# Optimization experiments

Measured on AMD Instinct MI355X. Metric: run time of the kernel, lower is better.

The kernel has to match this reference:

```python
import jax, jax.numpy as jnp
import numpy as np

WS = 8          # window size (Wh = Ww = 8)
N = WS * WS     # tokens per window = 64
DIM = 256
HEADS = 8
HEAD_DIM = DIM // HEADS
BW = 8192       # num_windows * batch


def _relative_position_index(ws: int) -> np.ndarray:
    ch, cw = np.meshgrid(np.arange(ws), np.arange(ws), indexing='ij')
    coords = np.stack([ch, cw]).reshape(2, -1)                 # (2, N)
    rel = coords[:, :, None] - coords[:, None, :]              # (2, N, N)
    rel = rel.transpose(1, 2, 0).astype(np.int32)              # (N, N, 2)
    rel[:, :, 0] += ws - 1
    rel[:, :, 1] += ws - 1
    rel[:, :, 0] *= 2 * ws - 1
    return rel.sum(-1)                                         # (N, N)


def setup_inputs() -> dict:
    key = jax.random.key(0)
    k1, k2, k3, k4, k5, k6 = jax.random.split(key, 6)
    table_size = (2 * WS - 1) * (2 * WS - 1)                   # 225
    return {
        'x': jax.random.normal(k1, (BW, N, DIM), dtype=jnp.float32),
        'w_qkv': jax.random.normal(k2, (3 * DIM, DIM), dtype=jnp.float32) * 0.02,
        'b_qkv': jax.random.normal(k3, (3 * DIM,), dtype=jnp.float32) * 0.02,
        'w_proj': jax.random.normal(k4, (DIM, DIM), dtype=jnp.float32) * 0.02,
        'b_proj': jax.random.normal(k5, (DIM,), dtype=jnp.float32) * 0.02,
        'rpb_table': jax.random.normal(k6, (table_size, HEADS), dtype=jnp.float32) * 0.02,
        'rpi': jnp.asarray(_relative_position_index(WS)),      # (N, N) int32
    }


def reference(x, w_qkv, b_qkv, w_proj, b_proj, rpb_table, rpi):
    b_, n, c = x.shape
    scale = HEAD_DIM ** (-0.5)
    qkv = x @ w_qkv.T + b_qkv                                  # (b_, n, 3c)
    qkv = qkv.reshape(b_, n, 3, HEADS, HEAD_DIM).transpose(2, 0, 3, 1, 4)
    q, k, v = qkv[0], qkv[1], qkv[2]                           # each (b_, H, n, d)
    attn = jnp.einsum('bhnd,bhmd->bhnm', q * scale, k)         # (b_, H, n, n)
    bias = rpb_table[rpi.reshape(-1)].reshape(n, n, HEADS)     # (n, n, H)
    attn = attn + bias.transpose(2, 0, 1)[None]                # + (1, H, n, n)
    attn = jax.nn.softmax(attn, axis=-1)
    out = jnp.einsum('bhnm,bhmd->bhnd', attn, v)               # (b_, H, n, d)
    out = out.transpose(0, 2, 1, 3).reshape(b_, n, c)
    return out @ w_proj.T + b_proj
```

## Files before the change

### kernel.cpp

```cpp
#include <hip/hip_runtime.h>
#include <hip/hip_bf16.h>

typedef __bf16 bf16x8 __attribute__((ext_vector_type(8)));
typedef float f32x4 __attribute__((ext_vector_type(4)));
typedef unsigned short u16;
typedef u16 u16x4 __attribute__((ext_vector_type(4)));
typedef u16 u16x8 __attribute__((ext_vector_type(8)));

__device__ __forceinline__ u16 bfbits(float f) {
  return __builtin_bit_cast(u16, (__bf16)f);
}

__global__ void wattn_prep(const float* __restrict__ wq, const float* __restrict__ wp,
                           const float* __restrict__ rpb, const int* __restrict__ rpi,
                           u16* __restrict__ wqb, u16* __restrict__ wpb,
                           float* __restrict__ biasb) {
  int i = blockIdx.x * blockDim.x + threadIdx.x;
  if (i < 196608) wqb[i] = bfbits(wq[i]);
  if (i < 65536)  wpb[i] = bfbits(wp[i]);
  if (i < 32768) {
    int h = i >> 12, nm = i & 4095;
    biasb[i] = rpb[rpi[nm] * 8 + h];
  }
}

__global__ __launch_bounds__(512, 4)
void wattn_main(const float* __restrict__ x,
                const u16* __restrict__ wq, const float* __restrict__ bq,
                const u16* __restrict__ wp, const float* __restrict__ bp,
                const float* __restrict__ bias,
                float* __restrict__ out) {
  extern __shared__ u16 sm[];
  u16* Xb = sm;
  u16* Vt = sm + 16896;

  const int b    = blockIdx.x;
  const int tid  = threadIdx.x;
  const int w    = tid >> 6;
  const int lane = tid & 63;
  const int g    = lane >> 4;
  const int li   = lane & 15;
  const int hc   = 32 * w;

  {
    const float4* xg = (const float4*)(x + (size_t)b * 16384);
    #pragma unroll
    for (int i = 0; i < 8; ++i) {
      int idx = tid + i * 512;
      float4 v = xg[idx];
      int n = idx >> 6, c = (idx & 63) * 4;
      u16x4 h;
      h[0] = bfbits(v.x); h[1] = bfbits(v.y); h[2] = bfbits(v.z); h[3] = bfbits(v.w);
      *(u16x4*)(Xb + n * 264 + c) = h;
    }
  }
  __syncthreads();

  const int xoff = li * 264 + 8 * g;

  f32x4 av[2][4];
  #pragma unroll
  for (int mt = 0; mt < 2; ++mt)
    #pragma unroll
    for (int nt = 0; nt < 4; ++nt) av[mt][nt] = f32x4{0,0,0,0};
  #pragma unroll 2
  for (int ks = 0; ks < 8; ++ks) {
    bf16x8 xb[4];
    #pragma unroll
    for (int nt = 0; nt < 4; ++nt)
      xb[nt] = *(const bf16x8*)(Xb + xoff + nt * (16 * 264) + 32 * ks);
    #pragma unroll
    for (int mt = 0; mt < 2; ++mt) {
      bf16x8 wf = *(const bf16x8*)(wq + (512 + hc + 16 * mt + li) * 256 + 32 * ks + 8 * g);
      #pragma unroll
      for (int nt = 0; nt < 4; ++nt)
        av[mt][nt] = __builtin_amdgcn_mfma_f32_16x16x32_bf16(wf, xb[nt], av[mt][nt], 0, 0, 0);
    }
  }
  {
    u16* VtW = Vt + w * 2304;
    #pragma unroll
    for (int mt = 0; mt < 2; ++mt)
      #pragma unroll
      for (int e = 0; e < 4; ++e) {
        float bb = bq[512 + hc + 16 * mt + 4 * g + e];
        #pragma unroll
        for (int nt = 0; nt < 4; ++nt)
          VtW[(16 * mt + 4 * g + e) * 72 + 16 * nt + li] = bfbits(av[mt][nt][e] + bb);
      }
  }
  __builtin_amdgcn_sched_barrier(0);

  const float scale = 0.17677669529663687f;
  bf16x8 qf[4];
  {
    f32x4 aq[2][4];
    #pragma unroll
    for (int mt = 0; mt < 2; ++mt)
      #pragma unroll
      for (int nt = 0; nt < 4; ++nt) aq[mt][nt] = f32x4{0,0,0,0};
    #pragma unroll 2
    for (int ks = 0; ks < 8; ++ks) {
      bf16x8 xb[4];
      #pragma unroll
      for (int nt = 0; nt < 4; ++nt)
        xb[nt] = *(const bf16x8*)(Xb + xoff + nt * (16 * 264) + 32 * ks);
      #pragma unroll
      for (int mt = 0; mt < 2; ++mt) {
        bf16x8 wf = *(const bf16x8*)(wq + (hc + 16 * mt + li) * 256 + 32 * ks + 8 * g);
        #pragma unroll
        for (int nt = 0; nt < 4; ++nt)
          aq[mt][nt] = __builtin_amdgcn_mfma_f32_16x16x32_bf16(wf, xb[nt], aq[mt][nt], 0, 0, 0);
      }
    }
    #pragma unroll
    for (int j = 0; j < 8; ++j) {
      int d = (j < 4) ? (4 * g + j) : (16 + 4 * g + (j - 4));
      float bb = bq[hc + d];
      #pragma unroll
      for (int t = 0; t < 4; ++t)
        qf[t][j] = (__bf16)(((j < 4 ? aq[0][t][j] : aq[1][t][j - 4]) + bb) * scale);
    }
  }
  __builtin_amdgcn_sched_barrier(0);

  bf16x8 kf[4];
  {
    f32x4 ak[2][4];
    #pragma unroll
    for (int mt = 0; mt < 2; ++mt)
      #pragma unroll
      for (int nt = 0; nt < 4; ++nt) ak[mt][nt] = f32x4{0,0,0,0};
    #pragma unroll 2
    for (int ks = 0; ks < 8; ++ks) {
      bf16x8 xb[4];
      #pragma unroll
      for (int nt = 0; nt < 4; ++nt)
        xb[nt] = *(const bf16x8*)(Xb + xoff + nt * (16 * 264) + 32 * ks);
      #pragma unroll
      for (int mt = 0; mt < 2; ++mt) {
        bf16x8 wf = *(const bf16x8*)(wq + (256 + hc + 16 * mt + li) * 256 + 32 * ks + 8 * g);
        #pragma unroll
        for (int nt = 0; nt < 4; ++nt)
          ak[mt][nt] = __builtin_amdgcn_mfma_f32_16x16x32_bf16(wf, xb[nt], ak[mt][nt], 0, 0, 0);
      }
    }
    #pragma unroll
    for (int j = 0; j < 8; ++j) {
      int d = (j < 4) ? (4 * g + j) : (16 + 4 * g + (j - 4));
      float bb = bq[256 + hc + d];
      #pragma unroll
      for (int t = 0; t < 4; ++t)
        kf[t][j] = (__bf16)((j < 4 ? ak[0][t][j] : ak[1][t][j - 4]) + bb);
    }
  }
  __builtin_amdgcn_sched_barrier(0);

  bf16x8 pa[4][2];
  {
    const float* bh = bias + w * 4096;
    #pragma unroll
    for (int ct = 0; ct < 4; ++ct) {
      f32x4 s4[4];
      #pragma unroll
      for (int rt = 0; rt < 4; ++rt)
        s4[rt] = __builtin_amdgcn_mfma_f32_16x16x32_bf16(kf[rt], qf[ct], f32x4{0,0,0,0}, 0, 0, 0);
      const float* bq_row = bh + (16 * ct + li) * 64 + 4 * g;
      float mx = -1e30f;
      #pragma unroll
      for (int rt = 0; rt < 4; ++rt) {
        f32x4 bv = *(const f32x4*)(bq_row + 16 * rt);
        #pragma unroll
        for (int e = 0; e < 4; ++e) {
          s4[rt][e] += bv[e];
          mx = fmaxf(mx, s4[rt][e]);
        }
      }
      mx = fmaxf(mx, __shfl_xor(mx, 16));
      mx = fmaxf(mx, __shfl_xor(mx, 32));
      float sum = 0.f;
      #pragma unroll
      for (int rt = 0; rt < 4; ++rt)
        #pragma unroll
        for (int e = 0; e < 4; ++e) {
          float p = __expf(s4[rt][e] - mx);
          s4[rt][e] = p;
          sum += p;
        }
      sum += __shfl_xor(sum, 16);
      sum += __shfl_xor(sum, 32);
      float rs = 1.0f / sum;
      #pragma unroll
      for (int kk = 0; kk < 2; ++kk)
        #pragma unroll
        for (int j = 0; j < 8; ++j)
          pa[ct][kk][j] = (__bf16)((j < 4 ? s4[2 * kk][j] : s4[2 * kk + 1][j - 4]) * rs);
      __builtin_amdgcn_sched_barrier(0);
    }
  }

  f32x4 o[4][2];
  #pragma unroll
  for (int mt = 0; mt < 4; ++mt)
    #pragma unroll
    for (int nt = 0; nt < 2; ++nt) o[mt][nt] = f32x4{0,0,0,0};
  {
    const u16* VtW = Vt + w * 2304;
    #pragma unroll
    for (int kk = 0; kk < 2; ++kk) {
      bf16x8 vb[2];
      #pragma unroll
      for (int nt = 0; nt < 2; ++nt) {
        const u16* row = VtW + (16 * nt + li) * 72;
        u16x4 lo = *(const u16x4*)(row + 32 * kk + 4 * g);
        u16x4 hi = *(const u16x4*)(row + 32 * kk + 16 + 4 * g);
        u16x8 cc;
        #pragma unroll
        for (int j = 0; j < 4; ++j) { cc[j] = lo[j]; cc[4 + j] = hi[j]; }
        vb[nt] = __builtin_bit_cast(bf16x8, cc);
      }
      #pragma unroll
      for (int mt = 0; mt < 4; ++mt)
        #pragma unroll
        for (int nt = 0; nt < 2; ++nt)
          o[mt][nt] = __builtin_amdgcn_mfma_f32_16x16x32_bf16(pa[mt][kk], vb[nt], o[mt][nt], 0, 0, 0);
    }
  }

  __syncthreads();
  u16* ao = sm;
  #pragma unroll
  for (int mt = 0; mt < 4; ++mt)
    #pragma unroll
    for (int nt = 0; nt < 2; ++nt)
      #pragma unroll
      for (int e = 0; e < 4; ++e)
        ao[(16 * mt + 4 * g + e) * 264 + hc + 16 * nt + li] = bfbits(o[mt][nt][e]);
  __syncthreads();

  f32x4 c2[4][2];
  #pragma unroll
  for (int rt = 0; rt < 4; ++rt)
    #pragma unroll
    for (int ct = 0; ct < 2; ++ct) c2[rt][ct] = f32x4{0,0,0,0};
  #pragma unroll 2
  for (int ks = 0; ks < 8; ++ks) {
    bf16x8 af[4];
    #pragma unroll
    for (int rt = 0; rt < 4; ++rt)
      af[rt] = *(const bf16x8*)(ao + xoff + rt * (16 * 264) + 32 * ks);
    bf16x8 wf[2];
    #pragma unroll
    for (int ct = 0; ct < 2; ++ct)
      wf[ct] = *(const bf16x8*)(wp + (32 * w + 16 * ct + li) * 256 + 32 * ks + 8 * g);
    #pragma unroll
    for (int rt = 0; rt < 4; ++rt)
      #pragma unroll
      for (int ct = 0; ct < 2; ++ct)
        c2[rt][ct] = __builtin_amdgcn_mfma_f32_16x16x32_bf16(af[rt], wf[ct], c2[rt][ct], 0, 0, 0);
  }
  {
    float* og = out + (size_t)b * 16384;
    #pragma unroll
    for (int ct = 0; ct < 2; ++ct) {
      int col = 32 * w + 16 * ct + li;
      float bpv = bp[col];
      #pragma unroll
      for (int rt = 0; rt < 4; ++rt)
        #pragma unroll
        for (int e = 0; e < 4; ++e)
          og[(16 * rt + 4 * g + e) * 256 + col] = c2[rt][ct][e] + bpv;
    }
  }
}

extern "C" void kernel_launch(void* const* d_in, const int* in_sizes, int n_in,
                              void* d_out, int out_size, void* d_ws, size_t ws_size,
                              hipStream_t stream) {
  const float* x   = (const float*)d_in[0];
  const float* wqv = (const float*)d_in[1];
  const float* bq  = (const float*)d_in[2];
  const float* wpr = (const float*)d_in[3];
  const float* bp  = (const float*)d_in[4];
  const float* rpb = (const float*)d_in[5];
  const int*   rpi = (const int*)d_in[6];
  float* out = (float*)d_out;

  u16*   wqb   = (u16*)d_ws;
  u16*   wpb   = wqb + 196608;
  float* biasb = (float*)(wpb + 65536);

  wattn_prep<<<384, 512, 0, stream>>>(wqv, wpr, rpb, rpi, wqb, wpb, biasb);

  const size_t smem = (16896 + 18432) * sizeof(u16);
  hipFuncSetAttribute(reinterpret_cast<const void*>(wattn_main),
                      hipFuncAttributeMaxDynamicSharedMemorySize, (int)smem);
  wattn_main<<<8192, 512, smem, stream>>>(x, wqb, bq, wpb, bp, biasb, out);
}
```

Before: 704.1 us.

## Keep V in registers via swapped MFMA operands, drop V LDS buffer

The V projection is now computed with X as the A operand and weights as B, so its accumulator layout matches the B-operand fragment needed by the P·V MFMA. V stays in registers instead of being written transposed to LDS and read back. This removes the V LDS buffer (shared memory per block roughly halves) and raises the launch-bounds occupancy hint from 4 to 6 blocks. It also moves the V projection after Q/K and removes a per-tile scheduling barrier in softmax. The risk is more register pressure, since V fragments stay live across the softmax, and possible spills under the tighter launch bound.

```diff
diff --git a/kernel.cpp b/kernel.cpp
--- a/kernel.cpp
+++ b/kernel.cpp
@@ -5,7 +5,6 @@
 typedef float f32x4 __attribute__((ext_vector_type(4)));
 typedef unsigned short u16;
 typedef u16 u16x4 __attribute__((ext_vector_type(4)));
-typedef u16 u16x8 __attribute__((ext_vector_type(8)));
 
 __device__ __forceinline__ u16 bfbits(float f) {
   return __builtin_bit_cast(u16, (__bf16)f);
@@ -24,7 +23,7 @@
   }
 }
 
-__global__ __launch_bounds__(512, 4)
+__global__ __launch_bounds__(512, 6)
 void wattn_main(const float* __restrict__ x,
                 const u16* __restrict__ wq, const float* __restrict__ bq,
                 const u16* __restrict__ wp, const float* __restrict__ bp,
@@ -32,7 +31,6 @@
                 float* __restrict__ out) {
   extern __shared__ u16 sm[];
   u16* Xb = sm;
-  u16* Vt = sm + 16896;
 
   const int b    = blockIdx.x;
   const int tid  = threadIdx.x;
@@ -57,41 +55,8 @@
   __syncthreads();
 
   const int xoff = li * 264 + 8 * g;
-
-  f32x4 av[2][4];
-  #pragma unroll
-  for (int mt = 0; mt < 2; ++mt)
-    #pragma unroll
-    for (int nt = 0; nt < 4; ++nt) av[mt][nt] = f32x4{0,0,0,0};
-  #pragma unroll 2
-  for (int ks = 0; ks < 8; ++ks) {
-    bf16x8 xb[4];
-    #pragma unroll
-    for (int nt = 0; nt < 4; ++nt)
-      xb[nt] = *(const bf16x8*)(Xb + xoff + nt * (16 * 264) + 32 * ks);
-    #pragma unroll
-    for (int mt = 0; mt < 2; ++mt) {
-      bf16x8 wf = *(const bf16x8*)(wq + (512 + hc + 16 * mt + li) * 256 + 32 * ks + 8 * g);
-      #pragma unroll
-      for (int nt = 0; nt < 4; ++nt)
-        av[mt][nt] = __builtin_amdgcn_mfma_f32_16x16x32_bf16(wf, xb[nt], av[mt][nt], 0, 0, 0);
-    }
-  }
-  {
-    u16* VtW = Vt + w * 2304;
-    #pragma unroll
-    for (int mt = 0; mt < 2; ++mt)
-      #pragma unroll
-      for (int e = 0; e < 4; ++e) {
-        float bb = bq[512 + hc + 16 * mt + 4 * g + e];
-        #pragma unroll
-        for (int nt = 0; nt < 4; ++nt)
-          VtW[(16 * mt + 4 * g + e) * 72 + 16 * nt + li] = bfbits(av[mt][nt][e] + bb);
-      }
-  }
-  __builtin_amdgcn_sched_barrier(0);
-
   const float scale = 0.17677669529663687f;
+
   bf16x8 qf[4];
   {
     f32x4 aq[2][4];
@@ -152,6 +117,39 @@
       #pragma unroll
       for (int t = 0; t < 4; ++t)
         kf[t][j] = (__bf16)((j < 4 ? ak[0][t][j] : ak[1][t][j - 4]) + bb);
+    }
+  }
+  __builtin_amdgcn_sched_barrier(0);
+
+  bf16x8 vb[2][2];
+  {
+    f32x4 av[4][2];
+    #pragma unroll
+    for (int mt = 0; mt < 4; ++mt)
+      #pragma unroll
+      for (int nt = 0; nt < 2; ++nt) av[mt][nt] = f32x4{0,0,0,0};
+    #pragma unroll 2
+    for (int ks = 0; ks < 8; ++ks) {
+      bf16x8 xb[4];
+      #pragma unroll
+      for (int mt = 0; mt < 4; ++mt)
+        xb[mt] = *(const bf16x8*)(Xb + xoff + mt * (16 * 264) + 32 * ks);
+      #pragma unroll
+      for (int nt = 0; nt < 2; ++nt) {
+        bf16x8 wf = *(const bf16x8*)(wq + (512 + hc + 16 * nt + li) * 256 + 32 * ks + 8 * g);
+        #pragma unroll
+        for (int mt = 0; mt < 4; ++mt)
+          av[mt][nt] = __builtin_amdgcn_mfma_f32_16x16x32_bf16(xb[mt], wf, av[mt][nt], 0, 0, 0);
+      }
+    }
+    #pragma unroll
+    for (int nt = 0; nt < 2; ++nt) {
+      float bb = bq[512 + hc + 16 * nt + li];
+      #pragma unroll
+      for (int kk = 0; kk < 2; ++kk)
+        #pragma unroll
+        for (int j = 0; j < 8; ++j)
+          vb[kk][nt][j] = (__bf16)((j < 4 ? av[2 * kk][nt][j] : av[2 * kk + 1][nt][j - 4]) + bb);
     }
   }
   __builtin_amdgcn_sched_barrier(0);
@@ -195,37 +193,22 @@
         #pragma unroll
         for (int j = 0; j < 8; ++j)
           pa[ct][kk][j] = (__bf16)((j < 4 ? s4[2 * kk][j] : s4[2 * kk + 1][j - 4]) * rs);
-      __builtin_amdgcn_sched_barrier(0);
-    }
-  }
+    }
+  }
+  __builtin_amdgcn_sched_barrier(0);
 
   f32x4 o[4][2];
   #pragma unroll
   for (int mt = 0; mt < 4; ++mt)
     #pragma unroll
     for (int nt = 0; nt < 2; ++nt) o[mt][nt] = f32x4{0,0,0,0};
-  {
-    const u16* VtW = Vt + w * 2304;
-    #pragma unroll
-    for (int kk = 0; kk < 2; ++kk) {
-      bf16x8 vb[2];
-      #pragma unroll
-      for (int nt = 0; nt < 2; ++nt) {
-        const u16* row = VtW + (16 * nt + li) * 72;
-        u16x4 lo = *(const u16x4*)(row + 32 * kk + 4 * g);
-        u16x4 hi = *(const u16x4*)(row + 32 * kk + 16 + 4 * g);
-        u16x8 cc;
-        #pragma unroll
-        for (int j = 0; j < 4; ++j) { cc[j] = lo[j]; cc[4 + j] = hi[j]; }
-        vb[nt] = __builtin_bit_cast(bf16x8, cc);
-      }
-      #pragma unroll
-      for (int mt = 0; mt < 4; ++mt)
-        #pragma unroll
-        for (int nt = 0; nt < 2; ++nt)
-          o[mt][nt] = __builtin_amdgcn_mfma_f32_16x16x32_bf16(pa[mt][kk], vb[nt], o[mt][nt], 0, 0, 0);
-    }
-  }
+  #pragma unroll
+  for (int kk = 0; kk < 2; ++kk)
+    #pragma unroll
+    for (int mt = 0; mt < 4; ++mt)
+      #pragma unroll
+      for (int nt = 0; nt < 2; ++nt)
+        o[mt][nt] = __builtin_amdgcn_mfma_f32_16x16x32_bf16(pa[mt][kk], vb[kk][nt], o[mt][nt], 0, 0, 0);
 
   __syncthreads();
   u16* ao = sm;
@@ -292,7 +275,7 @@
 
   wattn_prep<<<384, 512, 0, stream>>>(wqv, wpr, rpb, rpi, wqb, wpb, biasb);
 
-  const size_t smem = (16896 + 18432) * sizeof(u16);
+  const size_t smem = 16896 * sizeof(u16);
   hipFuncSetAttribute(reinterpret_cast<const void*>(wattn_main),
                       hipFuncAttributeMaxDynamicSharedMemorySize, (int)smem);
   wattn_main<<<8192, 512, smem, stream>>>(x, wqb, bq, wpb, bp, biasb, out);
```

New measurement: 1.165 ms. +65.4%, slower.

## Split fused window attention into attention and projection kernels via bf16 workspace

Applied to the files above, without the earlier changes.

Splits the single fused kernel into an attention kernel that writes a bf16 per-window output to global workspace and a separate projection kernel that reads it back. The attention kernel keeps V in registers instead of LDS, folds biases into accumulator initialization, and raises the occupancy target to 6 blocks per CU with smaller shared memory. This trades extra global traffic (a bf16 write and read of the intermediate, about 256 MB) for lower register and LDS pressure and higher occupancy. The original fused kernel remains as a fallback when the workspace is too small.

```diff
diff --git a/kernel.cpp b/kernel.cpp
--- a/kernel.cpp
+++ b/kernel.cpp
@@ -24,15 +24,13 @@
   }
 }
 
-__global__ __launch_bounds__(512, 4)
-void wattn_main(const float* __restrict__ x,
+__global__ __launch_bounds__(512, 6)
+void wattn_attn(const float* __restrict__ x,
                 const u16* __restrict__ wq, const float* __restrict__ bq,
-                const u16* __restrict__ wp, const float* __restrict__ bp,
                 const float* __restrict__ bias,
-                float* __restrict__ out) {
+                u16* __restrict__ ao) {
   extern __shared__ u16 sm[];
   u16* Xb = sm;
-  u16* Vt = sm + 16896;
 
   const int b    = blockIdx.x;
   const int tid  = threadIdx.x;
@@ -57,6 +55,231 @@
   __syncthreads();
 
   const int xoff = li * 264 + 8 * g;
+  const float scale = 0.17677669529663687f;
+
+  bf16x8 kf[4];
+  {
+    f32x4 ak[2][4];
+    #pragma unroll
+    for (int mt = 0; mt < 2; ++mt) {
+      f32x4 bkv = *(const f32x4*)(bq + 256 + hc + 16 * mt + 4 * g);
+      #pragma unroll
+      for (int nt = 0; nt < 4; ++nt) ak[mt][nt] = bkv;
+    }
+    #pragma unroll 1
+    for (int ks = 0; ks < 8; ++ks) {
+      bf16x8 xb[4];
+      #pragma unroll
+      for (int nt = 0; nt < 4; ++nt)
+        xb[nt] = *(const bf16x8*)(Xb + xoff + nt * (16 * 264) + 32 * ks);
+      #pragma unroll
+      for (int mt = 0; mt < 2; ++mt) {
+        bf16x8 wf = *(const bf16x8*)(wq + (256 + hc + 16 * mt + li) * 256 + 32 * ks + 8 * g);
+        #pragma unroll
+        for (int nt = 0; nt < 4; ++nt)
+          ak[mt][nt] = __builtin_amdgcn_mfma_f32_16x16x32_bf16(wf, xb[nt], ak[mt][nt], 0, 0, 0);
+      }
+    }
+    #pragma unroll
+    for (int j = 0; j < 8; ++j)
+      #pragma unroll
+      for (int t = 0; t < 4; ++t)
+        kf[t][j] = (__bf16)(j < 4 ? ak[0][t][j] : ak[1][t][j - 4]);
+  }
+  __builtin_amdgcn_sched_barrier(0);
+
+  bf16x8 vb[2][2];
+  #pragma unroll 1
+  for (int nt = 0; nt < 2; ++nt) {
+    f32x4 av[4];
+    {
+      float bb = bq[512 + hc + 16 * nt + li];
+      #pragma unroll
+      for (int mt = 0; mt < 4; ++mt) av[mt] = f32x4{bb, bb, bb, bb};
+    }
+    #pragma unroll 1
+    for (int ks = 0; ks < 8; ++ks) {
+      bf16x8 wf = *(const bf16x8*)(wq + (512 + hc + 16 * nt + li) * 256 + 32 * ks + 8 * g);
+      #pragma unroll
+      for (int mt = 0; mt < 4; ++mt) {
+        bf16x8 xb = *(const bf16x8*)(Xb + xoff + mt * (16 * 264) + 32 * ks);
+        av[mt] = __builtin_amdgcn_mfma_f32_16x16x32_bf16(xb, wf, av[mt], 0, 0, 0);
+      }
+    }
+    #pragma unroll
+    for (int kk = 0; kk < 2; ++kk)
+      #pragma unroll
+      for (int j = 0; j < 8; ++j)
+        vb[kk][nt][j] = (__bf16)(j < 4 ? av[2 * kk][j] : av[2 * kk + 1][j - 4]);
+    __builtin_amdgcn_sched_barrier(0);
+  }
+
+  bf16x8 qf[4];
+  #pragma unroll 1
+  for (int mt = 0; mt < 2; ++mt) {
+    f32x4 aq[4];
+    {
+      f32x4 bqv = *(const f32x4*)(bq + hc + 16 * mt + 4 * g);
+      #pragma unroll
+      for (int nt = 0; nt < 4; ++nt) aq[nt] = bqv;
+    }
+    #pragma unroll 1
+    for (int ks = 0; ks < 8; ++ks) {
+      bf16x8 wf = *(const bf16x8*)(wq + (hc + 16 * mt + li) * 256 + 32 * ks + 8 * g);
+      #pragma unroll
+      for (int nt = 0; nt < 4; ++nt) {
+        bf16x8 xb = *(const bf16x8*)(Xb + xoff + nt * (16 * 264) + 32 * ks);
+        aq[nt] = __builtin_amdgcn_mfma_f32_16x16x32_bf16(wf, xb, aq[nt], 0, 0, 0);
+      }
+    }
+    #pragma unroll
+    for (int t = 0; t < 4; ++t)
+      #pragma unroll
+      for (int j = 0; j < 4; ++j)
+        qf[t][4 * mt + j] = (__bf16)(aq[t][j] * scale);
+    __builtin_amdgcn_sched_barrier(0);
+  }
+
+  u16* aog = ao + (size_t)b * 16384;
+  const float* bh = bias + w * 4096;
+  #pragma unroll 1
+  for (int ct = 0; ct < 4; ++ct) {
+    const float* br = bh + (16 * ct + li) * 64 + 4 * g;
+    f32x4 s4[4];
+    #pragma unroll
+    for (int rt = 0; rt < 4; ++rt)
+      s4[rt] = __builtin_amdgcn_mfma_f32_16x16x32_bf16(kf[rt], qf[ct],
+                                                       *(const f32x4*)(br + 16 * rt), 0, 0, 0);
+    float mx = -1e30f;
+    #pragma unroll
+    for (int rt = 0; rt < 4; ++rt)
+      #pragma unroll
+      for (int e = 0; e < 4; ++e) mx = fmaxf(mx, s4[rt][e]);
+    mx = fmaxf(mx, __shfl_xor(mx, 16));
+    mx = fmaxf(mx, __shfl_xor(mx, 32));
+    float sum = 0.f;
+    #pragma unroll
+    for (int rt = 0; rt < 4; ++rt)
+      #pragma unroll
+      for (int e = 0; e < 4; ++e) {
+        float p = __expf(s4[rt][e] - mx);
+        s4[rt][e] = p;
+        sum += p;
+      }
+    sum += __shfl_xor(sum, 16);
+    sum += __shfl_xor(sum, 32);
+    float rs = 1.0f / sum;
+    bf16x8 pa0, pa1;
+    #pragma unroll
+    for (int j = 0; j < 8; ++j) {
+      pa0[j] = (__bf16)((j < 4 ? s4[0][j] : s4[1][j - 4]) * rs);
+      pa1[j] = (__bf16)((j < 4 ? s4[2][j] : s4[3][j - 4]) * rs);
+    }
+    #pragma unroll
+    for (int nt = 0; nt < 2; ++nt) {
+      f32x4 o = __builtin_amdgcn_mfma_f32_16x16x32_bf16(pa0, vb[0][nt], f32x4{0, 0, 0, 0}, 0, 0, 0);
+      o = __builtin_amdgcn_mfma_f32_16x16x32_bf16(pa1, vb[1][nt], o, 0, 0, 0);
+      #pragma unroll
+      for (int e = 0; e < 4; ++e)
+        aog[(16 * ct + 4 * g + e) * 256 + hc + 16 * nt + li] = bfbits(o[e]);
+    }
+    __builtin_amdgcn_sched_barrier(0);
+  }
+}
+
+__global__ __launch_bounds__(512, 6)
+void wattn_proj(const u16* __restrict__ ao, const u16* __restrict__ wp,
+                const float* __restrict__ bp, float* __restrict__ out) {
+  extern __shared__ u16 sm[];
+  const int b    = blockIdx.x;
+  const int tid  = threadIdx.x;
+  const int w    = tid >> 6;
+  const int lane = tid & 63;
+  const int g    = lane >> 4;
+  const int li   = lane & 15;
+
+  {
+    const u16x8* src = (const u16x8*)(ao + (size_t)b * 16384);
+    #pragma unroll
+    for (int i = 0; i < 4; ++i) {
+      int idx = tid + i * 512;
+      u16x8 v = src[idx];
+      int row = idx >> 5, c = (idx & 31) * 8;
+      *(u16x8*)(sm + row * 264 + c) = v;
+    }
+  }
+  __syncthreads();
+
+  const int xoff = li * 264 + 8 * g;
+  f32x4 c2[4][2];
+  #pragma unroll
+  for (int c = 0; c < 2; ++c) {
+    float bb = bp[32 * w + 16 * c + li];
+    #pragma unroll
+    for (int rt = 0; rt < 4; ++rt) c2[rt][c] = f32x4{bb, bb, bb, bb};
+  }
+  #pragma unroll 1
+  for (int ks = 0; ks < 8; ++ks) {
+    bf16x8 af[4];
+    #pragma unroll
+    for (int rt = 0; rt < 4; ++rt)
+      af[rt] = *(const bf16x8*)(sm + xoff + rt * (16 * 264) + 32 * ks);
+    #pragma unroll
+    for (int c = 0; c < 2; ++c) {
+      bf16x8 wf = *(const bf16x8*)(wp + (32 * w + 16 * c + li) * 256 + 32 * ks + 8 * g);
+      #pragma unroll
+      for (int rt = 0; rt < 4; ++rt)
+        c2[rt][c] = __builtin_amdgcn_mfma_f32_16x16x32_bf16(af[rt], wf, c2[rt][c], 0, 0, 0);
+    }
+  }
+  {
+    float* og = out + (size_t)b * 16384;
+    #pragma unroll
+    for (int c = 0; c < 2; ++c) {
+      int col = 32 * w + 16 * c + li;
+      #pragma unroll
+      for (int rt = 0; rt < 4; ++rt)
+        #pragma unroll
+        for (int e = 0; e < 4; ++e)
+          og[(16 * rt + 4 * g + e) * 256 + col] = c2[rt][c][e];
+    }
+  }
+}
+
+__global__ __launch_bounds__(512, 4)
+void wattn_fused(const float* __restrict__ x,
+                 const u16* __restrict__ wq, const float* __restrict__ bq,
+                 const u16* __restrict__ wp, const float* __restrict__ bp,
+                 const float* __restrict__ bias,
+                 float* __restrict__ out) {
+  extern __shared__ u16 sm[];
+  u16* Xb = sm;
+  u16* Vt = sm + 16896;
+
+  const int b    = blockIdx.x;
+  const int tid  = threadIdx.x;
+  const int w    = tid >> 6;
+  const int lane = tid & 63;
+  const int g    = lane >> 4;
+  const int li   = lane & 15;
+  const int hc   = 32 * w;
+
+  {
+    const float4* xg = (const float4*)(x + (size_t)b * 16384);
+    #pragma unroll
+    for (int i = 0; i < 8; ++i) {
+      int idx = tid + i * 512;
+      float4 v = xg[idx];
+      int n = idx >> 6, c = (idx & 63) * 4;
+      u16x4 h;
+      h[0] = bfbits(v.x); h[1] = bfbits(v.y); h[2] = bfbits(v.z); h[3] = bfbits(v.w);
+      *(u16x4*)(Xb + n * 264 + c) = h;
+    }
+  }
+  __syncthreads();
+
+  const int xoff = li * 264 + 8 * g;
+  const float scale = 0.17677669529663687f;
 
   f32x4 av[2][4];
   #pragma unroll
@@ -91,7 +314,6 @@
   }
   __builtin_amdgcn_sched_barrier(0);
 
-  const float scale = 0.17677669529663687f;
   bf16x8 qf[4];
   {
     f32x4 aq[2][4];
@@ -208,7 +430,7 @@
     const u16* VtW = Vt + w * 2304;
     #pragma unroll
     for (int kk = 0; kk < 2; ++kk) {
-      bf16x8 vb[2];
+      bf16x8 vbf[2];
       #pragma unroll
       for (int nt = 0; nt < 2; ++nt) {
         const u16* row = VtW + (16 * nt + li) * 72;
@@ -217,13 +439,13 @@
         u16x8 cc;
         #pragma unroll
         for (int j = 0; j < 4; ++j) { cc[j] = lo[j]; cc[4 + j] = hi[j]; }
-        vb[nt] = __builtin_bit_cast(bf16x8, cc);
+        vbf[nt] = __builtin_bit_cast(bf16x8, cc);
       }
       #pragma unroll
       for (int mt = 0; mt < 4; ++mt)
         #pragma unroll
         for (int nt = 0; nt < 2; ++nt)
-          o[mt][nt] = __builtin_amdgcn_mfma_f32_16x16x32_bf16(pa[mt][kk], vb[nt], o[mt][nt], 0, 0, 0);
+          o[mt][nt] = __builtin_amdgcn_mfma_f32_16x16x32_bf16(pa[mt][kk], vbf[nt], o[mt][nt], 0, 0, 0);
     }
   }
 
@@ -289,11 +511,19 @@
   u16*   wqb   = (u16*)d_ws;
   u16*   wpb   = wqb + 196608;
   float* biasb = (float*)(wpb + 65536);
+  u16*   ao    = (u16*)((char*)d_ws + 655360);
 
   wattn_prep<<<384, 512, 0, stream>>>(wqv, wpr, rpb, rpi, wqb, wpb, biasb);
 
-  const size_t smem = (16896 + 18432) * sizeof(u16);
-  hipFuncSetAttribute(reinterpret_cast<const void*>(wattn_main),
-                      hipFuncAttributeMaxDynamicSharedMemorySize, (int)smem);
-  wattn_main<<<8192, 512, smem, stream>>>(x, wqb, bq, wpb, bp, biasb, out);
+  const size_t need = 655360u + 268435456u;
+  if (ws_size >= need) {
+    const size_t smemA = 16896 * sizeof(u16);
+    wattn_attn<<<8192, 512, smemA, stream>>>(x, wqb, bq, biasb, ao);
+    wattn_proj<<<8192, 512, smemA, stream>>>(ao, wpb, bp, out);
+  } else {
+    const size_t smemF = (16896 + 18432) * sizeof(u16);
+    hipFuncSetAttribute(reinterpret_cast<const void*>(wattn_fused),
+                        hipFuncAttributeMaxDynamicSharedMemorySize, (int)smemF);
+    wattn_fused<<<8192, 512, smemF, stream>>>(x, wqb, bq, wpb, bp, biasb, out);
+  }
 }
```

New measurement: 937.8 us. 33.2% more time.
